# Kernel optimization log

Measured on AMD Instinct MI355X. Metric: run time of the kernel, lower is better.

The kernel has to match this reference:

```python
import jax, jax.numpy as jnp
import numpy as np

N_HEAD = 12
N_EMBD = 768


def setup_inputs() -> dict:
    key = jax.random.key(0)
    k1, k2, k3 = jax.random.split(key, 3)
    B, T, C = 4, 2048, N_EMBD
    x = jax.random.normal(k1, (B, T, C), dtype=jnp.float32)
    # nn.Linear weights stored as [out, in]; apply as x @ W.T
    scale_attn = 1.0 / np.sqrt(C)
    w_attn = jax.random.normal(k2, (3 * C, C), dtype=jnp.float32) * scale_attn
    w_proj = jax.random.normal(k3, (C, C), dtype=jnp.float32) * scale_attn
    return {"x": x, "w_attn": w_attn, "w_proj": w_proj}


def reference(x, w_attn, w_proj):
    B, T, C = x.shape
    H, D = N_HEAD, C // N_HEAD
    qkv = jnp.einsum("btc,fc->btf", x, w_attn)          # [B,T,3C]
    q, k, v = jnp.split(qkv, 3, axis=-1)
    # [B,T,C] -> [B,H,T,D]
    q = q.reshape(B, T, H, D).transpose(0, 2, 1, 3)
    k = k.reshape(B, T, H, D).transpose(0, 2, 1, 3)
    v = v.reshape(B, T, H, D).transpose(0, 2, 1, 3)
    scores = jnp.einsum("bhqd,bhkd->bhqk", q, k) / jnp.sqrt(jnp.asarray(D, x.dtype))
    attn = jax.nn.softmax(scores, axis=-1)
    y = jnp.einsum("bhqk,bhkd->bhqd", attn, v)          # [B,H,T,D]
    y = y.transpose(0, 2, 1, 3).reshape(B, T, C)
    return jnp.einsum("btc,oc->bto", y, w_proj)
```

## Files before the change

### kernel.cpp

```cpp
#include <hip/hip_runtime.h>
#include <stdint.h>

typedef unsigned short u16;
typedef uint32_t u32;
typedef __attribute__((ext_vector_type(8))) short short8;
typedef __attribute__((ext_vector_type(4))) float f32x4;
typedef __attribute__((ext_vector_type(16))) float f32x16;

static constexpr int T_SEQ = 2048;
static constexpr int C_EMB = 768;
static constexpr int N_HD  = 12;
static constexpr int D_HD  = 64;
static constexpr int N_BH  = 48;

#define MFMA16(a, b, c) __builtin_amdgcn_mfma_f32_16x16x32_bf16((a), (b), (c), 0, 0, 0)
#define MFMA32(a, b, c) __builtin_amdgcn_mfma_f32_32x32x16_bf16((a), (b), (c), 0, 0, 0)

#if __has_builtin(__builtin_amdgcn_exp2f)
#define EXP2(x) __builtin_amdgcn_exp2f(x)
#else
#define EXP2(x) exp2f(x)
#endif

__device__ __forceinline__ u16 f2bf(float f) {
  union { float f; u32 u; } v; v.f = f;
  u32 r = v.u + 0x7FFFu + ((v.u >> 16) & 1u);
  return (u16)(r >> 16);
}
__device__ __forceinline__ float bf2f(u16 h) {
  union { u32 u; float f; } v; v.u = ((u32)h) << 16; return v.f;
}
__device__ __forceinline__ u32 pack_bf16(float lo, float hi) {
  return (u32)f2bf(lo) | ((u32)f2bf(hi) << 16);
}

__device__ __forceinline__ void gload_lds16(const void* g, void* l) {
  __builtin_amdgcn_global_load_lds((const __attribute__((address_space(1))) void*)g,
                                   (__attribute__((address_space(3))) void*)l, 16, 0, 0);
}

__device__ __forceinline__ int swz(int r, int kb) {
  return r * 128 + (kb ^ ((r & 7) << 4));
}

__global__ void split_kernel(const float* __restrict__ src, u16* __restrict__ hi,
                             u16* __restrict__ lo, int n4) {
  int i = blockIdx.x * blockDim.x + threadIdx.x;
  int stride = gridDim.x * blockDim.x;
  for (; i < n4; i += stride) {
    float4 v = ((const float4*)src)[i];
    ushort4 H;
    H.x = f2bf(v.x); H.y = f2bf(v.y); H.z = f2bf(v.z); H.w = f2bf(v.w);
    ((ushort4*)hi)[i] = H;
    if (lo) {
      ushort4 L;
      L.x = f2bf(v.x - bf2f(H.x)); L.y = f2bf(v.y - bf2f(H.y));
      L.z = f2bf(v.z - bf2f(H.z)); L.w = f2bf(v.w - bf2f(H.w));
      ((ushort4*)lo)[i] = L;
    }
  }
}

template <int EPI, int PASSES, int MINW>
__global__ __launch_bounds__(256, MINW) void gemm_nt(
    const u16* __restrict__ Ah, const u16* __restrict__ Al,
    const u16* __restrict__ Bh, const u16* __restrict__ Bl, int K,
    u16* __restrict__ qg, u16* __restrict__ kg, u16* __restrict__ vtg,
    float* __restrict__ outp, int ldout) {
  constexpr int NT = (PASSES == 2) ? 3 : 4;
  __shared__ __align__(16) char lds[NT * 16384];
  char* LA_h = lds;
  char* LA_l = lds + 16384;
  char* LB_h = lds + 32768;
  char* LB_l = lds + ((NT == 4) ? 49152 : 32768);
  const int tid = threadIdx.x, lane = tid & 63, w = tid >> 6;
  const int g = lane >> 4, c16 = lane & 15;
  const int wr = w >> 1, wc = w & 1;
  const int nwg = gridDim.x * gridDim.y;
  const int id = blockIdx.y * gridDim.x + blockIdx.x;
  const int sw = (id & 7) * (nwg >> 3) + (id >> 3);
  const int m0 = (sw / gridDim.x) * 128, n0 = (sw % gridDim.x) * 128;
  f32x4 acc[4][4] = {};

  for (int k0 = 0; k0 < K; k0 += 64) {
    __syncthreads();
#pragma unroll
    for (int tile = 0; tile < NT; tile++) {
      const u16* src = (tile == 0) ? Ah : (tile == 1) ? Al : (tile == 2) ? Bh : Bl;
      const int row0 = (tile < 2) ? m0 : n0;
      char* dst = lds + tile * 16384;
#pragma unroll
      for (int i = 0; i < 4; i++) {
        int c = tid + 256 * i;
        int r = c >> 3;
        int sp = (c & 7) ^ (r & 7);
        gload_lds16(src + (size_t)(row0 + r) * K + k0 + sp * 8,
                    dst + w * 1024 + i * 4096);
      }
    }
    __syncthreads();
#pragma unroll
    for (int ks = 0; ks < 2; ks++) {
      const int kb = ks * 64 + g * 16;
      short8 aH[4], aL[4], bH[4], bL[4];
#pragma unroll
      for (int mf = 0; mf < 4; mf++) {
        int r = wr * 64 + mf * 16 + c16;
        aH[mf] = *(const short8*)(LA_h + swz(r, kb));
        aL[mf] = *(const short8*)(LA_l + swz(r, kb));
      }
#pragma unroll
      for (int nf = 0; nf < 4; nf++) {
        int r = wc * 64 + nf * 16 + c16;
        bH[nf] = *(const short8*)(LB_h + swz(r, kb));
        if (PASSES == 3) bL[nf] = *(const short8*)(LB_l + swz(r, kb));
      }
#pragma unroll
      for (int mf = 0; mf < 4; mf++)
#pragma unroll
        for (int nf = 0; nf < 4; nf++) {
          acc[mf][nf] = MFMA16(aH[mf], bH[nf], acc[mf][nf]);
          acc[mf][nf] = MFMA16(aL[mf], bH[nf], acc[mf][nf]);
          if (PASSES == 3) acc[mf][nf] = MFMA16(aH[mf], bL[nf], acc[mf][nf]);
        }
    }
  }

#pragma unroll
  for (int mf = 0; mf < 4; mf++)
#pragma unroll
    for (int nf = 0; nf < 4; nf++) {
      if (EPI == 0) {
        int col = n0 + wc * 64 + nf * 16 + c16;
        int p = (col >= 2 * C_EMB) ? 2 : (col >= C_EMB ? 1 : 0);
        int rem = col - p * C_EMB;
        int h = rem >> 6, d = rem & 63;
        int rowb = m0 + wr * 64 + mf * 16 + g * 4;
        int b = rowb >> 11, t0 = rowb & (T_SEQ - 1);
        int bhh = b * N_HD + h;
        if (p == 2) {
          ushort4 V4;
#pragma unroll
          for (int jj = 0; jj < 4; jj++) (&V4.x)[jj] = f2bf(acc[mf][nf][jj]);
          *(ushort4*)(vtg + ((size_t)bhh * D_HD + d) * T_SEQ + t0) = V4;
        } else {
          u16* dst = (p == 0) ? qg : kg;
          float scl = (p == 0) ? 0.18033688f : 1.0f;
#pragma unroll
          for (int jj = 0; jj < 4; jj++)
            dst[((size_t)bhh * T_SEQ + t0 + jj) * D_HD + d] = f2bf(acc[mf][nf][jj] * scl);
        }
      } else {
#pragma unroll
        for (int jj = 0; jj < 4; jj++) {
          int row = m0 + wr * 64 + mf * 16 + g * 4 + jj;
          int col = n0 + wc * 64 + nf * 16 + c16;
          outp[(size_t)row * ldout + col] = acc[mf][nf][jj];
        }
      }
    }
}

__global__ __launch_bounds__(256, 3) void fa_kernel(
    const u16* __restrict__ qg, const u16* __restrict__ kg,
    const u16* __restrict__ vtg, u16* __restrict__ yh, u16* __restrict__ yl) {
  __shared__ __align__(16) char lds[32768];
  char* LK = lds;
  char* LV = lds + 16384;
  const int tid = threadIdx.x, lane = tid & 63, w = tid >> 6;
  const int r31 = lane & 31, hi = lane >> 5;
  const int bh = blockIdx.x, qb = blockIdx.y;
  const size_t kvbase = (size_t)bh * T_SEQ * D_HD;

  const u16* qrow = qg + kvbase + (size_t)(qb * 128 + w * 32 + r31) * D_HD + hi * 8;
  short8 qf[4];
#pragma unroll
  for (int ks = 0; ks < 4; ks++) qf[ks] = *(const short8*)(qrow + ks * 16);

  f32x16 yac[2] = {};
  float lsum = 0.f;

  for (int kt = 0; kt < T_SEQ / 128; kt++) {
    const int kv0 = kt * 128;
    __syncthreads();
#pragma unroll
    for (int i = 0; i < 4; i++) {
      int c = tid + 256 * i;
      int kr = c >> 3, ksl = (c & 7) ^ (kr & 7);
      gload_lds16(kg + kvbase + (size_t)(kv0 + kr) * D_HD + ksl * 8,
                  LK + w * 1024 + i * 4096);
      int vd = c >> 4, vsl = (c & 15) ^ (vd & 15);
      gload_lds16(vtg + kvbase + (size_t)vd * T_SEQ + kv0 + vsl * 8,
                  LV + w * 1024 + i * 4096);
    }
    __syncthreads();

    f32x16 p[4];
#pragma unroll
    for (int nb = 0; nb < 4; nb++) {
      f32x16 s = {};
#pragma unroll
      for (int ks = 0; ks < 4; ks++) {
        int row = nb * 32 + r31;
        short8 kf = *(const short8*)(LK + row * 128 + (((2 * ks + hi) ^ (row & 7)) << 4));
        s = MFMA32(kf, qf[ks], s);
      }
      p[nb] = s;
    }

#pragma unroll
    for (int nb = 0; nb < 4; nb++)
#pragma unroll
      for (int rr = 0; rr < 16; rr++) p[nb][rr] = EXP2(p[nb][rr]);
    {
      f32x16 t0 = p[0] + p[1];
      f32x16 t1 = p[2] + p[3];
      t0 = t0 + t1;
      float a = ((t0[0] + t0[1]) + (t0[2] + t0[3])) + ((t0[4] + t0[5]) + (t0[6] + t0[7]));
      float b = ((t0[8] + t0[9]) + (t0[10] + t0[11])) + ((t0[12] + t0[13]) + (t0[14] + t0[15]));
      lsum += a + b;
    }

#pragma unroll
    for (int nb = 0; nb < 4; nb++) {
      u32 wd[8];
#pragma unroll
      for (int i = 0; i < 8; i++)
        wd[i] = pack_bf16(p[nb][2 * i], p[nb][2 * i + 1]);
#pragma unroll
      for (int q4 = 0; q4 < 2; q4++) {
        union { u32 u[4]; short8 s8; } pu;
        pu.u[0] = wd[q4 * 4 + 0]; pu.u[1] = wd[q4 * 4 + 1];
        pu.u[2] = wd[q4 * 4 + 2]; pu.u[3] = wd[q4 * 4 + 3];
        const int slot = 4 * nb + 2 * q4;
#pragma unroll
        for (int nd = 0; nd < 2; nd++) {
          int d = nd * 32 + r31;
          union { uint2 u2[2]; short8 s8; } vu;
          vu.u2[0] = *(const uint2*)(LV + d * 256 + ((slot ^ (d & 15)) << 4) + 8 * hi);
          vu.u2[1] = *(const uint2*)(LV + d * 256 + (((slot + 1) ^ (d & 15)) << 4) + 8 * hi);
          yac[nd] = MFMA32(vu.s8, pu.s8, yac[nd]);
        }
      }
    }
  }

  lsum += __shfl_xor(lsum, 32);
  float inv = 1.0f / lsum;
  const int b = bh / N_HD, hh = bh % N_HD;
  const int t = qb * 128 + w * 32 + r31;
  const size_t ybase = ((size_t)b * T_SEQ + t) * C_EMB + hh * D_HD;
#pragma unroll
  for (int nd = 0; nd < 2; nd++)
#pragma unroll
    for (int rq = 0; rq < 4; rq++) {
      int d0 = nd * 32 + rq * 8 + hi * 4;
      ushort4 H, L;
#pragma unroll
      for (int jj = 0; jj < 4; jj++) {
        float v = yac[nd][rq * 4 + jj] * inv;
        u16 hv = f2bf(v);
        (&H.x)[jj] = hv;
        (&L.x)[jj] = f2bf(v - bf2f(hv));
      }
      *(ushort4*)(yh + ybase + d0) = H;
      *(ushort4*)(yl + ybase + d0) = L;
    }
}

extern "C" void kernel_launch(void* const* d_in, const int* in_sizes, int n_in,
                              void* d_out, int out_size, void* d_ws, size_t ws_size,
                              hipStream_t stream) {
  (void)in_sizes; (void)n_in; (void)out_size;
  const float* x      = (const float*)d_in[0];
  const float* w_attn = (const float*)d_in[1];
  const float* w_proj = (const float*)d_in[2];
  float* out = (float*)d_out;

  const size_t NX  = (size_t)4 * T_SEQ * C_EMB;
  const size_t NWA = (size_t)3 * C_EMB * C_EMB;
  const size_t NWP = (size_t)C_EMB * C_EMB;
  const size_t NQ  = (size_t)N_BH * T_SEQ * D_HD;

  u16* ws = (u16*)d_ws;
  size_t off = 0;
  u16* XH  = ws + off; off += NX;   u16* XL  = ws + off; off += NX;
  u16* WAH = ws + off; off += NWA;
  u16* WPH = ws + off; off += NWP;  u16* WPL = ws + off; off += NWP;
  u16* QB  = ws + off; off += NQ;
  u16* KB  = ws + off; off += NQ;
  u16* VT  = ws + off; off += NQ;
  u16* YH  = ws + off; off += NX;   u16* YL  = ws + off; off += NX;
  if (ws_size < off * sizeof(u16)) return;

  auto blks = [](size_t n4) {
    size_t b = (n4 + 255) / 256; return (unsigned)(b > 2048 ? 2048 : b);
  };
  split_kernel<<<blks(NX / 4), 256, 0, stream>>>(x, XH, XL, (int)(NX / 4));
  split_kernel<<<blks(NWA / 4), 256, 0, stream>>>(w_attn, WAH, nullptr, (int)(NWA / 4));
  split_kernel<<<blks(NWP / 4), 256, 0, stream>>>(w_proj, WPH, WPL, (int)(NWP / 4));

  gemm_nt<0, 2, 3><<<dim3(3 * C_EMB / 128, 4 * T_SEQ / 128), 256, 0, stream>>>(
      XH, XL, WAH, nullptr, C_EMB, QB, KB, VT, nullptr, 0);

  fa_kernel<<<dim3(N_BH, T_SEQ / 128), 256, 0, stream>>>(QB, KB, VT, YH, YL);

  gemm_nt<1, 3, 2><<<dim3(C_EMB / 128, 4 * T_SEQ / 128), 256, 0, stream>>>(
      YH, YL, WPH, WPL, C_EMB, nullptr, nullptr, nullptr, out, C_EMB);
}
```

Baseline: 247.6 us.

## Use single-pass bf16 QKV GEMM, precompute LDS pointers, cheaper packing in attention

Result: faster. 211.5 us (-14.6%).

```diff
diff --git a/kernel.cpp b/kernel.cpp
--- a/kernel.cpp
+++ b/kernel.cpp
@@ -30,8 +30,9 @@
 __device__ __forceinline__ float bf2f(u16 h) {
   union { u32 u; float f; } v; v.u = ((u32)h) << 16; return v.f;
 }
-__device__ __forceinline__ u32 pack_bf16(float lo, float hi) {
-  return (u32)f2bf(lo) | ((u32)f2bf(hi) << 16);
+__device__ __forceinline__ u32 pack2bf(float a, float b) {
+  union { float f; u32 u; } x, y; x.f = a; y.f = b;
+  return __byte_perm(x.u + 0x8000u, y.u + 0x8000u, 0x7632);
 }
 
 __device__ __forceinline__ void gload_lds16(const void* g, void* l) {
@@ -67,12 +68,13 @@
     const u16* __restrict__ Bh, const u16* __restrict__ Bl, int K,
     u16* __restrict__ qg, u16* __restrict__ kg, u16* __restrict__ vtg,
     float* __restrict__ outp, int ldout) {
-  constexpr int NT = (PASSES == 2) ? 3 : 4;
+  constexpr int NA = (PASSES >= 2) ? 2 : 1;
+  constexpr int NT = NA + ((PASSES == 3) ? 2 : 1);
   __shared__ __align__(16) char lds[NT * 16384];
   char* LA_h = lds;
   char* LA_l = lds + 16384;
-  char* LB_h = lds + 32768;
-  char* LB_l = lds + ((NT == 4) ? 49152 : 32768);
+  char* LB_h = lds + NA * 16384;
+  char* LB_l = lds + (NA + 1) * 16384;
   const int tid = threadIdx.x, lane = tid & 63, w = tid >> 6;
   const int g = lane >> 4, c16 = lane & 15;
   const int wr = w >> 1, wc = w & 1;
@@ -86,8 +88,9 @@
     __syncthreads();
 #pragma unroll
     for (int tile = 0; tile < NT; tile++) {
-      const u16* src = (tile == 0) ? Ah : (tile == 1) ? Al : (tile == 2) ? Bh : Bl;
-      const int row0 = (tile < 2) ? m0 : n0;
+      const u16* src = (tile < NA) ? ((tile == 0) ? Ah : Al)
+                                   : ((tile == NA) ? Bh : Bl);
+      const int row0 = (tile < NA) ? m0 : n0;
       char* dst = lds + tile * 16384;
 #pragma unroll
       for (int i = 0; i < 4; i++) {
@@ -107,7 +110,7 @@
       for (int mf = 0; mf < 4; mf++) {
         int r = wr * 64 + mf * 16 + c16;
         aH[mf] = *(const short8*)(LA_h + swz(r, kb));
-        aL[mf] = *(const short8*)(LA_l + swz(r, kb));
+        if (PASSES >= 2) aL[mf] = *(const short8*)(LA_l + swz(r, kb));
       }
 #pragma unroll
       for (int nf = 0; nf < 4; nf++) {
@@ -120,7 +123,7 @@
 #pragma unroll
         for (int nf = 0; nf < 4; nf++) {
           acc[mf][nf] = MFMA16(aH[mf], bH[nf], acc[mf][nf]);
-          acc[mf][nf] = MFMA16(aL[mf], bH[nf], acc[mf][nf]);
+          if (PASSES >= 2) acc[mf][nf] = MFMA16(aL[mf], bH[nf], acc[mf][nf]);
           if (PASSES == 3) acc[mf][nf] = MFMA16(aH[mf], bL[nf], acc[mf][nf]);
         }
     }
@@ -142,7 +145,8 @@
           ushort4 V4;
 #pragma unroll
           for (int jj = 0; jj < 4; jj++) (&V4.x)[jj] = f2bf(acc[mf][nf][jj]);
-          *(ushort4*)(vtg + ((size_t)bhh * D_HD + d) * T_SEQ + t0) = V4;
+          int t0p = (t0 & ~12) | ((t0 & 4) << 1) | ((t0 & 8) >> 1);
+          *(ushort4*)(vtg + ((size_t)bhh * D_HD + d) * T_SEQ + t0p) = V4;
         } else {
           u16* dst = (p == 0) ? qg : kg;
           float scl = (p == 0) ? 0.18033688f : 1.0f;
@@ -177,8 +181,21 @@
 #pragma unroll
   for (int ks = 0; ks < 4; ks++) qf[ks] = *(const short8*)(qrow + ks * 16);
 
+  const int eK = r31 & 7, eV = r31 & 15;
+  const char* pK[4];
+#pragma unroll
+  for (int ks = 0; ks < 4; ks++)
+    pK[ks] = LK + r31 * 128 + ((hi ^ (eK & 1)) << 4) + (((ks << 5) ^ ((eK >> 1) << 5)));
+  const char* pV[2][8];
+#pragma unroll
+  for (int nd = 0; nd < 2; nd++)
+#pragma unroll
+    for (int kk = 0; kk < 8; kk++)
+      pV[nd][kk] = LV + (nd * 32 + r31) * 256 + ((hi ^ (eV & 1)) << 4) +
+                   (((kk << 5) ^ ((eV >> 1) << 5)));
+
   f32x16 yac[2] = {};
-  float lsum = 0.f;
+  f32x16 lacc = {};
 
   for (int kt = 0; kt < T_SEQ / 128; kt++) {
     const int kv0 = kt * 128;
@@ -201,8 +218,7 @@
       f32x16 s = {};
 #pragma unroll
       for (int ks = 0; ks < 4; ks++) {
-        int row = nb * 32 + r31;
-        short8 kf = *(const short8*)(LK + row * 128 + (((2 * ks + hi) ^ (row & 7)) << 4));
+        short8 kf = *(const short8*)(pK[ks] + nb * 4096);
         s = MFMA32(kf, qf[ks], s);
       }
       p[nb] = s;
@@ -212,39 +228,37 @@
     for (int nb = 0; nb < 4; nb++)
 #pragma unroll
       for (int rr = 0; rr < 16; rr++) p[nb][rr] = EXP2(p[nb][rr]);
-    {
-      f32x16 t0 = p[0] + p[1];
-      f32x16 t1 = p[2] + p[3];
-      t0 = t0 + t1;
-      float a = ((t0[0] + t0[1]) + (t0[2] + t0[3])) + ((t0[4] + t0[5]) + (t0[6] + t0[7]));
-      float b = ((t0[8] + t0[9]) + (t0[10] + t0[11])) + ((t0[12] + t0[13]) + (t0[14] + t0[15]));
-      lsum += a + b;
-    }
+    lacc += (p[0] + p[1]) + (p[2] + p[3]);
 
 #pragma unroll
     for (int nb = 0; nb < 4; nb++) {
       u32 wd[8];
 #pragma unroll
       for (int i = 0; i < 8; i++)
-        wd[i] = pack_bf16(p[nb][2 * i], p[nb][2 * i + 1]);
+        wd[i] = pack2bf(p[nb][2 * i], p[nb][2 * i + 1]);
 #pragma unroll
       for (int q4 = 0; q4 < 2; q4++) {
         union { u32 u[4]; short8 s8; } pu;
         pu.u[0] = wd[q4 * 4 + 0]; pu.u[1] = wd[q4 * 4 + 1];
         pu.u[2] = wd[q4 * 4 + 2]; pu.u[3] = wd[q4 * 4 + 3];
-        const int slot = 4 * nb + 2 * q4;
+        const int kk = nb * 2 + q4;
 #pragma unroll
         for (int nd = 0; nd < 2; nd++) {
-          int d = nd * 32 + r31;
-          union { uint2 u2[2]; short8 s8; } vu;
-          vu.u2[0] = *(const uint2*)(LV + d * 256 + ((slot ^ (d & 15)) << 4) + 8 * hi);
-          vu.u2[1] = *(const uint2*)(LV + d * 256 + (((slot + 1) ^ (d & 15)) << 4) + 8 * hi);
-          yac[nd] = MFMA32(vu.s8, pu.s8, yac[nd]);
+          short8 vf = *(const short8*)(pV[nd][kk]);
+          yac[nd] = MFMA32(vf, pu.s8, yac[nd]);
         }
       }
     }
   }
 
+  float lsum;
+  {
+    float a = ((lacc[0] + lacc[1]) + (lacc[2] + lacc[3])) +
+              ((lacc[4] + lacc[5]) + (lacc[6] + lacc[7]));
+    float b = ((lacc[8] + lacc[9]) + (lacc[10] + lacc[11])) +
+              ((lacc[12] + lacc[13]) + (lacc[14] + lacc[15]));
+    lsum = a + b;
+  }
   lsum += __shfl_xor(lsum, 32);
   float inv = 1.0f / lsum;
   const int b = bh / N_HD, hh = bh % N_HD;
@@ -284,7 +298,7 @@
 
   u16* ws = (u16*)d_ws;
   size_t off = 0;
-  u16* XH  = ws + off; off += NX;   u16* XL  = ws + off; off += NX;
+  u16* XH  = ws + off; off += NX;
   u16* WAH = ws + off; off += NWA;
   u16* WPH = ws + off; off += NWP;  u16* WPL = ws + off; off += NWP;
   u16* QB  = ws + off; off += NQ;
@@ -296,12 +310,12 @@
   auto blks = [](size_t n4) {
     size_t b = (n4 + 255) / 256; return (unsigned)(b > 2048 ? 2048 : b);
   };
-  split_kernel<<<blks(NX / 4), 256, 0, stream>>>(x, XH, XL, (int)(NX / 4));
+  split_kernel<<<blks(NX / 4), 256, 0, stream>>>(x, XH, nullptr, (int)(NX / 4));
   split_kernel<<<blks(NWA / 4), 256, 0, stream>>>(w_attn, WAH, nullptr, (int)(NWA / 4));
   split_kernel<<<blks(NWP / 4), 256, 0, stream>>>(w_proj, WPH, WPL, (int)(NWP / 4));
 
-  gemm_nt<0, 2, 3><<<dim3(3 * C_EMB / 128, 4 * T_SEQ / 128), 256, 0, stream>>>(
-      XH, XL, WAH, nullptr, C_EMB, QB, KB, VT, nullptr, 0);
+  gemm_nt<0, 1, 3><<<dim3(3 * C_EMB / 128, 4 * T_SEQ / 128), 256, 0, stream>>>(
+      XH, nullptr, WAH, nullptr, C_EMB, QB, KB, VT, nullptr, 0);
 
   fa_kernel<<<dim3(N_BH, T_SEQ / 128), 256, 0, stream>>>(QB, KB, VT, YH, YL);
 
```
